# Performance work log

Hardware: AMD Instinct MI355X
Metric: run time of the kernel (lower is better)

Reference implementation:

```python
import jax, jax.numpy as jnp
import numpy as np

EPS_OT = 0.05
SINK_ITERS = 3
HEADS = 8


def _l2norm(x, axis):
    n = jnp.sqrt(jnp.sum(x * x, axis=axis, keepdims=True))
    return x / jnp.maximum(n, 1e-12)


def _conv(x, w, b, pad):
    y = jax.lax.conv_general_dilated(x, w, (1, 1), [(pad, pad), (pad, pad)],
                                     dimension_numbers=('NCHW', 'OIHW', 'NCHW'))
    return y + b[None, :, None, None]


def _bn(x, g, b):
    # BatchNorm2d in training mode: batch statistics over (B,H,W)
    m = jnp.mean(x, axis=(0, 2, 3), keepdims=True)
    v = jnp.var(x, axis=(0, 2, 3), keepdims=True)
    return (x - m) / jnp.sqrt(v + 1e-5) * g[None, :, None, None] + b[None, :, None, None]


def setup_inputs() -> dict:
    key = jax.random.key(0)
    ks = jax.random.split(key, 16)
    B, C, H, W = 2, 256, 64, 64
    TXT = 512
    rn = lambda k, shp, s=0.02: jax.random.normal(k, shp, dtype=jnp.float32) * s
    return {
        'img_feat': jax.random.normal(ks[0], (B, C, H, W), jnp.float32),
        'txt_feat': jax.random.normal(ks[1], (B, TXT), jnp.float32),
        'density_map': jax.random.uniform(ks[2], (B, 1, H, W), dtype=jnp.float32),
        'tp_w': rn(ks[3], (C, TXT)), 'tp_b': jnp.zeros((C,), jnp.float32),
        'wq': rn(ks[4], (C, C)), 'bq': jnp.zeros((C,), jnp.float32),
        'wk': rn(ks[5], (C, C)), 'bk': jnp.zeros((C,), jnp.float32),
        'wv': rn(ks[6], (C, C)), 'bv': jnp.zeros((C,), jnp.float32),
        'wo': rn(ks[7], (C, C)), 'bo': jnp.zeros((C,), jnp.float32),
        'ln_g': jnp.ones((C,), jnp.float32), 'ln_b': jnp.zeros((C,), jnp.float32),
        'op_w': rn(ks[8], (C, C, 1, 1)), 'op_b': jnp.zeros((C,), jnp.float32),
        'hm1_w': rn(ks[9], (C // 2, C, 3, 3)), 'hm1_b': jnp.zeros((C // 2,), jnp.float32),
        'hm_bn_g': jnp.ones((C // 2,), jnp.float32), 'hm_bn_b': jnp.zeros((C // 2,), jnp.float32),
        'hm2_w': rn(ks[10], (2, C // 2, 1, 1)), 'hm2_b': jnp.zeros((2,), jnp.float32),
        'hv1_w': rn(ks[11], (C // 2, C, 3, 3)), 'hv1_b': jnp.zeros((C // 2,), jnp.float32),
        'hv_bn_g': jnp.ones((C // 2,), jnp.float32), 'hv_bn_b': jnp.zeros((C // 2,), jnp.float32),
        'hv2_w': rn(ks[12], (2, C // 2, 1, 1)), 'hv2_b': jnp.zeros((2,), jnp.float32),
        'temperature': jnp.ones((1,), jnp.float32) * 0.07,
    }


def reference(img_feat, txt_feat, density_map, tp_w, tp_b, wq, bq, wk, bk, wv, bv,
              wo, bo, ln_g, ln_b, op_w, op_b, hm1_w, hm1_b, hm_bn_g, hm_bn_b,
              hm2_w, hm2_b, hv1_w, hv1_b, hv_bn_g, hv_bn_b, hv2_w, hv2_b, temperature):
    B, C, H, W = img_feat.shape
    N = H * W
    dh = C // HEADS

    # text projection -> single token [B,1,C]
    txt_emb = (txt_feat @ tp_w.T + tp_b)[:, None, :]
    img_flat = img_feat.reshape(B, C, N).transpose(0, 2, 1)  # [B,N,C]

    # multihead cross-attention, kv length 1
    q = (img_flat @ wq.T + bq).reshape(B, N, HEADS, dh)
    k = (txt_emb @ wk.T + bk).reshape(B, 1, HEADS, dh)
    v = (txt_emb @ wv.T + bv).reshape(B, 1, HEADS, dh)
    scores = jnp.einsum('bnhd,bmhd->bhnm', q, k) / np.float32(np.sqrt(dh))
    w_attn = jax.nn.softmax(scores, axis=-1)
    attn_out = jnp.einsum('bhnm,bmhd->bnhd', w_attn, v).reshape(B, N, C) @ wo.T + bo

    # residual + layernorm
    x = img_flat + attn_out
    mu = jnp.mean(x, axis=-1, keepdims=True)
    var = jnp.var(x, axis=-1, keepdims=True)
    source = (x - mu) / jnp.sqrt(var + 1e-5) * ln_g + ln_b  # [B,N,C]
    mod_img = source.transpose(0, 2, 1).reshape(B, C, H, W)

    # target marginal from density map
    target = jax.nn.relu(density_map.reshape(B, N)) + 1e-6
    q_marg = target / jnp.sum(target, axis=1, keepdims=True)

    # source marginal from cosine similarity to text
    img_n = _l2norm(mod_img, 1)
    txt_n = _l2norm(txt_emb[:, 0, :], 1)  # [B,C]
    cos = jnp.einsum('bchw,bc->bhw', img_n, txt_n).reshape(B, N)
    temp = jnp.maximum(temperature, 0.01)
    p_marg = jax.nn.softmax(cos / temp, axis=1)

    # Sinkhorn OT over NxN cosine cost
    sn = _l2norm(source, 2)
    sim = jnp.einsum('bnc,bmc->bnm', sn, sn)
    K = jnp.exp(-(1.0 - sim) / EPS_OT)
    u = jnp.ones_like(p_marg)
    vv = jnp.ones_like(q_marg)
    for _ in range(SINK_ITERS):
        vv = q_marg / (jnp.einsum('bnm,bn->bm', K, u) + 1e-8)
        u = p_marg / (jnp.einsum('bnm,bm->bn', K, vv) + 1e-8)
    T = u[:, :, None] * K * vv[:, None, :]
    fused = jnp.einsum('bnm,bnc->bmc', T, source)  # T^T @ source

    fused_feat = fused.transpose(0, 2, 1).reshape(B, C, H, W)
    out_feat = img_feat + _conv(fused_feat, op_w, op_b, 0)

    hm = _conv(jax.nn.relu(_bn(_conv(out_feat, hm1_w, hm1_b, 1), hm_bn_g, hm_bn_b)), hm2_w, hm2_b, 0)
    hv = _conv(jax.nn.relu(_bn(_conv(out_feat, hv1_w, hv1_b, 1), hv_bn_g, hv_bn_b)), hv2_w, hv2_b, 0)
    return (out_feat, hm, hv)
```

## Files before the change

kernel.cpp:

```cpp
#include <hip/hip_runtime.h>

#define B_ 2
#define C_ 256
#define N_ 4096
#define TXT_ 512
#define CH_ 128
#define TN 32
#define KSPLIT 4
#define PXR 4224
#define PXPAD 96
#define PXTOT (PXR + 2 * PXPAD)
#define L2E 28.853900817779268f

typedef unsigned short u16;
typedef unsigned char u8;
typedef __attribute__((ext_vector_type(8))) short short8;
typedef __attribute__((ext_vector_type(4))) float f32x4;
typedef __attribute__((ext_vector_type(2))) float f32x2;

__device__ __forceinline__ float bf2f(u16 v){
  union { unsigned u; float f; } w; w.u = ((unsigned)v) << 16; return w.f;
}
__device__ __forceinline__ u16 f2bf(float f){
  union { float f; unsigned u; } w; w.f = f;
  unsigned r = w.u + 0x7fffu + ((w.u >> 16) & 1u);
  return (u16)(r >> 16);
}

#define MFMA_BF16(a,b,c) __builtin_amdgcn_mfma_f32_16x16x32_bf16(a,b,c,0,0,0)

__device__ __forceinline__ void stage_tile(const u16* __restrict__ g, int stride, u16* lds, int t)
{
  #pragma unroll
  for (int q = 0; q < 4; q++){
    int e = q * 256 + t;
    int row = e >> 3;
    int slot = e & 7;
    const u16* gp = g + (size_t)row * stride + ((slot ^ (row & 7)) << 3);
    u16* lp = lds + (size_t)e * 8;
    __builtin_amdgcn_global_load_lds((const __attribute__((address_space(1))) void*)gp,
                                     (__attribute__((address_space(3))) void*)lp, 16, 0, 0);
  }
}

__device__ __forceinline__ void stage_tile512_256(const u16* __restrict__ g, int stride, u16* lds, int t)
{
  #pragma unroll
  for (int q = 0; q < 4; q++){
    int e = q * 512 + t;
    int row = e >> 3;
    int slot = e & 7;
    const u16* gp = g + (size_t)row * stride + ((slot ^ (row & 7)) << 3);
    u16* lp = lds + (size_t)e * 8;
    __builtin_amdgcn_global_load_lds((const __attribute__((address_space(1))) void*)gp,
                                     (__attribute__((address_space(3))) void*)lp, 16, 0, 0);
  }
}

__device__ __forceinline__ short8 frag_ld(const u16* lds, int row, int slot)
{
  return *(const short8*)(lds + row * 64 + ((slot ^ (row & 7)) << 3));
}

__global__ __launch_bounds__(256) void k_text(
    const float* __restrict__ txt, const float* __restrict__ tpw,
    const float* __restrict__ tpb, const float* __restrict__ wv,
    const float* __restrict__ bv, const float* __restrict__ wo,
    const float* __restrict__ bo,
    float* __restrict__ txt_emb, float* __restrict__ attn_c, float* __restrict__ txt_n)
{
  int b = blockIdx.x, t = threadIdx.x;
  __shared__ float te[C_], vs[C_], red[C_];
  const float* tb = txt + b * TXT_;
  const float* wr = tpw + (size_t)t * TXT_;
  float s = 0.f;
  for (int j = 0; j < TXT_; j++) s += tb[j] * wr[j];
  s += tpb[t];
  te[t] = s;
  txt_emb[b * C_ + t] = s;
  __syncthreads();
  float sv = 0.f;
  const float* wvr = wv + (size_t)t * C_;
  for (int j = 0; j < C_; j++) sv += te[j] * wvr[j];
  sv += bv[t];
  vs[t] = sv;
  __syncthreads();
  float sa = 0.f;
  const float* wor = wo + (size_t)t * C_;
  for (int j = 0; j < C_; j++) sa += vs[j] * wor[j];
  sa += bo[t];
  attn_c[b * C_ + t] = sa;
  red[t] = te[t] * te[t];
  __syncthreads();
  for (int o = 128; o > 0; o >>= 1){ if (t < o) red[t] += red[t + o]; __syncthreads(); }
  float nrm = sqrtf(red[0]);
  float inv = 1.f / fmaxf(nrm, 1e-12f);
  txt_n[b * C_ + t] = te[t] * inv;
}

__global__ __launch_bounds__(256) void k_source(
    const float* __restrict__ img, const float* __restrict__ attn_c,
    const float* __restrict__ ln_g, const float* __restrict__ ln_b,
    const float* __restrict__ txt_n,
    u16* __restrict__ srcT, u16* __restrict__ snb, float* __restrict__ cosv)
{
  int b = blockIdx.y;
  int n0 = blockIdx.x * TN;
  int t = threadIdx.x;
  __shared__ float x[C_][TN + 1];
  __shared__ float ps[8][TN];
  __shared__ float ps2[8][TN];
  __shared__ float ac_s[C_], g_s[C_], bb_s[C_], tn_s[C_];
  __shared__ float mean_s[TN], rstd_s[TN], rn_s[TN];
  ac_s[t] = attn_c[b * C_ + t];
  g_s[t]  = ln_g[t];
  bb_s[t] = ln_b[t];
  tn_s[t] = txt_n[b * C_ + t];
  const float* ib = img + (size_t)b * C_ * N_ + n0;
  for (int k = 0; k < TN; k++){
    int e = t + k * 256;
    int c = e >> 5, nn = e & 31;
    x[c][nn] = ib[(size_t)c * N_ + nn];
  }
  __syncthreads();
  for (int k = 0; k < TN; k++){
    int e = t + k * 256;
    int c = e >> 5, nn = e & 31;
    x[c][nn] += ac_s[c];
  }
  __syncthreads();
  {
    int p = t >> 5, nn = t & 31;
    float s1 = 0.f, s2 = 0.f;
    for (int j = 0; j < 32; j++){
      float v = x[p + 8 * j][nn];
      s1 += v; s2 += v * v;
    }
    ps[p][nn] = s1; ps2[p][nn] = s2;
  }
  __syncthreads();
  if (t < TN){
    float S1 = 0.f, S2 = 0.f;
    for (int pp = 0; pp < 8; pp++){ S1 += ps[pp][t]; S2 += ps2[pp][t]; }
    float mean = S1 * (1.f / C_);
    float var = S2 * (1.f / C_) - mean * mean;
    mean_s[t] = mean;
    rstd_s[t] = rsqrtf(var + 1e-5f);
  }
  __syncthreads();
  for (int k = 0; k < TN; k++){
    float sval = (x[t][k] - mean_s[k]) * rstd_s[k] * g_s[t] + bb_s[t];
    x[t][k] = sval;
  }
  for (int kq = 0; kq < TN; kq += 4){
    ushort4 pkv;
    pkv.x = f2bf(x[t][kq + 0]);
    pkv.y = f2bf(x[t][kq + 1]);
    pkv.z = f2bf(x[t][kq + 2]);
    pkv.w = f2bf(x[t][kq + 3]);
    *reinterpret_cast<ushort4*>(&srcT[(size_t)(b * C_ + t) * N_ + n0 + kq]) = pkv;
  }
  __syncthreads();
  {
    int p = t >> 5, nn = t & 31;
    float s2 = 0.f, sd = 0.f;
    for (int j = 0; j < 32; j++){
      int c = p + 8 * j;
      float v = x[c][nn];
      s2 += v * v; sd += v * tn_s[c];
    }
    ps[p][nn] = s2; ps2[p][nn] = sd;
  }
  __syncthreads();
  if (t < TN){
    float S2 = 0.f, SD = 0.f;
    for (int pp = 0; pp < 8; pp++){ S2 += ps[pp][t]; SD += ps2[pp][t]; }
    float nrm = sqrtf(S2);
    float rn = 1.f / fmaxf(nrm, 1e-12f);
    rn_s[t] = rn;
    cosv[(b << 12) + n0 + t] = SD * rn;
  }
  __syncthreads();
  for (int k = 0; k < TN; k++){
    snb[(size_t)((b << 12) + n0 + k) * C_ + t] = f2bf(x[t][k] * rn_s[k]);
  }
}

__global__ __launch_bounds__(256) void k_qmarg(const float* __restrict__ dens, float* __restrict__ q){
  int b = blockIdx.x, t = threadIdx.x;
  __shared__ float red[256];
  const float* d = dens + (size_t)b * N_;
  float s = 0.f;
  for (int n = t; n < N_; n += 256) s += fmaxf(d[n], 0.f) + 1e-6f;
  red[t] = s; __syncthreads();
  for (int o = 128; o > 0; o >>= 1){ if (t < o) red[t] += red[t + o]; __syncthreads(); }
  float inv = 1.f / red[0];
  for (int n = t; n < N_; n += 256) q[b * N_ + n] = (fmaxf(d[n], 0.f) + 1e-6f) * inv;
}

__global__ __launch_bounds__(256) void k_pmarg(const float* __restrict__ cosv,
    const float* __restrict__ temp_p, float* __restrict__ p){
  int b = blockIdx.x, t = threadIdx.x;
  __shared__ float red[256];
  float temp = fmaxf(temp_p[0], 0.01f);
  float inv_t = 1.f / temp;
  const float* cb = cosv + (size_t)b * N_;
  float m = -1e30f;
  for (int n = t; n < N_; n += 256) m = fmaxf(m, cb[n] * inv_t);
  red[t] = m; __syncthreads();
  for (int o = 128; o > 0; o >>= 1){ if (t < o) red[t] = fmaxf(red[t], red[t + o]); __syncthreads(); }
  m = red[0]; __syncthreads();
  float s = 0.f;
  for (int n = t; n < N_; n += 256) s += expf(cb[n] * inv_t - m);
  red[t] = s; __syncthreads();
  for (int o = 128; o > 0; o >>= 1){ if (t < o) red[t] += red[t + o]; __syncthreads(); }
  float invs = 1.f / red[0];
  for (int n = t; n < N_; n += 256) p[b * N_ + n] = expf(cb[n] * inv_t - m) * invs;
}

__global__ __launch_bounds__(256) void k_zero(float* __restrict__ p, int n){
  int i = blockIdx.x * 256 + threadIdx.x;
  if (i < n) p[i] = 0.f;
}

__global__ __launch_bounds__(256) void k_kgen(
    const u16* __restrict__ snb, u8* __restrict__ Kp, float* __restrict__ colsum)
{
  int b = blockIdx.z;
  int m0 = blockIdx.x << 7, n0 = blockIdx.y << 7;
  int t = threadIdx.x;
  int lane = t & 63, w = t >> 6;
  int wr = w >> 1, wc = w & 1;
  __shared__ __align__(16) u16 shbuf[128 * 128];
  u16* Al = shbuf;
  u16* Bl = shbuf + 128 * 64;
  __shared__ float cs[128];
  if (t < 128) cs[t] = 0.f;
  f32x4 zero = {0.f, 0.f, 0.f, 0.f};
  f32x4 acc[4][4];
  #pragma unroll
  for (int i = 0; i < 4; i++){
    #pragma unroll
    for (int j = 0; j < 4; j++) acc[i][j] = zero;
  }
  const u16* sb = snb + (size_t)b * N_ * C_;
  const u16* ga = sb + (size_t)m0 * C_;
  const u16* gb = sb + (size_t)n0 * C_;
  for (int kt = 0; kt < C_; kt += 64){
    stage_tile(ga + kt, C_, Al, t);
    stage_tile(gb + kt, C_, Bl, t);
    __syncthreads();
    #pragma unroll
    for (int kh = 0; kh < 2; kh++){
      short8 af[4], bfv[4];
      #pragma unroll
      for (int i = 0; i < 4; i++){
        af[i]  = frag_ld(Al, wr * 64 + i * 16 + (lane & 15), kh * 4 + (lane >> 4));
        bfv[i] = frag_ld(Bl, wc * 64 + i * 16 + (lane & 15), kh * 4 + (lane >> 4));
      }
      #pragma unroll
      for (int i = 0; i < 4; i++){
        #pragma unroll
        for (int j = 0; j < 4; j++)
          acc[i][j] = MFMA_BF16(af[i], bfv[j], acc[i][j]);
      }
    }
    __syncthreads();
  }
  u8* CtT = (u8*)shbuf;
  #pragma unroll
  for (int j = 0; j < 4; j++){
    int col = wc * 64 + j * 16 + (lane & 15);
    float csum = 0.f;
    #pragma unroll
    for (int i = 0; i < 4; i++){
      int rb = wr * 64 + i * 16 + (lane >> 4) * 4;
      float e0 = __builtin_amdgcn_exp2f(fmaf(acc[i][j][0], L2E, -L2E));
      float e1 = __builtin_amdgcn_exp2f(fmaf(acc[i][j][1], L2E, -L2E));
      float e2 = __builtin_amdgcn_exp2f(fmaf(acc[i][j][2], L2E, -L2E));
      float e3 = __builtin_amdgcn_exp2f(fmaf(acc[i][j][3], L2E, -L2E));
      int pk = __builtin_amdgcn_cvt_pk_fp8_f32(e0, e1, 0, false);
      pk = __builtin_amdgcn_cvt_pk_fp8_f32(e2, e3, pk, true);
      f32x2 d0 = __builtin_amdgcn_cvt_pk_f32_fp8(pk, false);
      f32x2 d1 = __builtin_amdgcn_cvt_pk_f32_fp8(pk, true);
      csum += (d0.x + d0.y) + (d1.x + d1.y);
      int wq = rb >> 2;
      *reinterpret_cast<unsigned*>(CtT + col * 128 + ((wq ^ ((col & 7) << 2)) << 2)) = (unsigned)pk;
    }
    atomicAdd(&cs[col], csum);
  }
  __syncthreads();
  u8* Kb = Kp + (size_t)b * N_ * N_;
  for (int e = t; e < 1024; e += 256){
    int row = e >> 3, un = e & 7;
    uint4 v = *(const uint4*)(CtT + row * 128 + ((un ^ (row & 7)) << 4));
    *reinterpret_cast<uint4*>(&Kb[(size_t)(n0 + row) * N_ + m0 + (un << 4)]) = v;
  }
  if (t < 128) atomicAdd(&colsum[b * N_ + n0 + t], cs[t]);
}

__global__ __launch_bounds__(256) void k_div(
    const float* __restrict__ marg, const float* __restrict__ denom, float* __restrict__ outp){
  int i = blockIdx.x * 256 + threadIdx.x;
  if (i < B_ * N_) outp[i] = marg[i] / (denom[i] + 1e-8f);
}

__global__ __launch_bounds__(256) void k_mv(
    const u8* __restrict__ Kp, const float* __restrict__ x,
    const float* __restrict__ marg, float* __restrict__ outp)
{
  int r0 = blockIdx.x * 8;
  int b = r0 >> 12;
  int t = threadIdx.x, w = t >> 6, lane = t & 63;
  __shared__ __align__(16) float xs[N_];
  const float* xb = x + b * N_;
  for (int i = t; i < N_ / 4; i += 256)
    reinterpret_cast<float4*>(xs)[i] = reinterpret_cast<const float4*>(xb)[i];
  __syncthreads();
  int r = r0 + w * 2;
  const u8* Kr0 = Kp + (size_t)b * N_ * N_ + (size_t)(r & (N_ - 1)) * N_;
  const u8* Kr1 = Kr0 + N_;
  float acc0 = 0.f, acc1 = 0.f;
  #pragma unroll
  for (int p = 0; p < 4; p++){
    int idx = p * 1024 + lane * 16;
    uint4 a = *reinterpret_cast<const uint4*>(Kr0 + idx);
    uint4 c = *reinterpret_cast<const uint4*>(Kr1 + idx);
    #pragma unroll
    for (int q = 0; q < 4; q++){
      unsigned aw = (q == 0) ? a.x : (q == 1) ? a.y : (q == 2) ? a.z : a.w;
      unsigned cw = (q == 0) ? c.x : (q == 1) ? c.y : (q == 2) ? c.z : c.w;
      float4 xv = *reinterpret_cast<const float4*>(xs + idx + q * 4);
      f32x2 al = __builtin_amdgcn_cvt_pk_f32_fp8((int)aw, false);
      f32x2 ah = __builtin_amdgcn_cvt_pk_f32_fp8((int)aw, true);
      f32x2 cl = __builtin_amdgcn_cvt_pk_f32_fp8((int)cw, false);
      f32x2 ch = __builtin_amdgcn_cvt_pk_f32_fp8((int)cw, true);
      acc0 += al.x * xv.x + al.y * xv.y + ah.x * xv.z + ah.y * xv.w;
      acc1 += cl.x * xv.x + cl.y * xv.y + ch.x * xv.z + ch.y * xv.w;
    }
  }
  for (int o = 32; o > 0; o >>= 1){
    acc0 += __shfl_down(acc0, o);
    acc1 += __shfl_down(acc1, o);
  }
  if (lane == 0){
    outp[r] = marg[r] / (acc0 + 1e-8f);
    outp[r + 1] = marg[r + 1] / (acc1 + 1e-8f);
  }
}

__global__ __launch_bounds__(256) void k_uscale(
    const u16* __restrict__ srcT, const float* __restrict__ uu, u16* __restrict__ usrcT)
{
  int i = blockIdx.x * 256 + threadIdx.x;
  int n8 = i & (N_ / 8 - 1);
  int row = i >> 9;
  int b = row >> 8;
  const u16* s = srcT + (size_t)row * N_ + n8 * 8;
  short8 v = *reinterpret_cast<const short8*>(s);
  const float* ub = uu + b * N_ + n8 * 8;
  short8 o;
  #pragma unroll
  for (int q = 0; q < 8; q++) o[q] = (short)f2bf(bf2f((u16)v[q]) * ub[q]);
  *reinterpret_cast<short8*>(usrcT + (size_t)row * N_ + n8 * 8) = o;
}

__global__ __launch_bounds__(512) void k_full(
    const u8* __restrict__ Kp, const u16* __restrict__ usrcT,
    const float* __restrict__ vvv,
    u16* __restrict__ p0, u16* __restrict__ p1,
    u16* __restrict__ p2, u16* __restrict__ p3)
{
  int m0 = blockIdx.x << 6;
  int b = blockIdx.z >> 2, ks = blockIdx.z & 3;
  int t = threadIdx.x, lane = t & 63, w = t >> 6;
  __shared__ __align__(16) u16 shbuf[64 * 64 + 256 * 64];
  __shared__ float vsm[64];
  u16* Al = shbuf;
  u16* Bl = shbuf + 64 * 64;
  if (t < 64) vsm[t] = vvv[b * N_ + m0 + t];
  f32x4 zero = {0.f, 0.f, 0.f, 0.f};
  f32x4 acc[4][2];
  #pragma unroll
  for (int i = 0; i < 4; i++){
    #pragma unroll
    for (int j = 0; j < 2; j++) acc[i][j] = zero;
  }
  const u8* ka = Kp + (size_t)b * N_ * N_ + (size_t)m0 * N_ + ks * (N_ / KSPLIT);
  const u16* ub = usrcT + (size_t)b * C_ * N_ + ks * (N_ / KSPLIT);
  for (int kt = 0; kt < N_ / KSPLIT; kt += 64){
    {
      int row = t >> 3, slot = t & 7;
      const u8* gp = ka + (size_t)row * N_ + kt + ((slot ^ (row & 7)) << 3);
      uint2 v8 = *reinterpret_cast<const uint2*>(gp);
      f32x2 q0 = __builtin_amdgcn_cvt_pk_f32_fp8((int)v8.x, false);
      f32x2 q1 = __builtin_amdgcn_cvt_pk_f32_fp8((int)v8.x, true);
      f32x2 q2 = __builtin_amdgcn_cvt_pk_f32_fp8((int)v8.y, false);
      f32x2 q3 = __builtin_amdgcn_cvt_pk_f32_fp8((int)v8.y, true);
      union { short8 s; unsigned u[4]; } o;
      asm("v_cvt_pk_bf16_f32 %0, %1, %2" : "=v"(o.u[0]) : "v"(q0.x), "v"(q0.y));
      asm("v_cvt_pk_bf16_f32 %0, %1, %2" : "=v"(o.u[1]) : "v"(q1.x), "v"(q1.y));
      asm("v_cvt_pk_bf16_f32 %0, %1, %2" : "=v"(o.u[2]) : "v"(q2.x), "v"(q2.y));
      asm("v_cvt_pk_bf16_f32 %0, %1, %2" : "=v"(o.u[3]) : "v"(q3.x), "v"(q3.y));
      *reinterpret_cast<short8*>(Al + (size_t)t * 8) = o.s;
    }
    stage_tile512_256(ub + kt, N_, Bl, t);
    __syncthreads();
    #pragma unroll
    for (int kh = 0; kh < 2; kh++){
      short8 af[4], bfv[2];
      #pragma unroll
      for (int i = 0; i < 4; i++)
        af[i] = frag_ld(Al, i * 16 + (lane & 15), kh * 4 + (lane >> 4));
      #pragma unroll
      for (int j = 0; j < 2; j++)
        bfv[j] = frag_ld(Bl, w * 32 + j * 16 + (lane & 15), kh * 4 + (lane >> 4));
      #pragma unroll
      for (int i = 0; i < 4; i++){
        #pragma unroll
        for (int j = 0; j < 2; j++)
          acc[i][j] = MFMA_BF16(af[i], bfv[j], acc[i][j]);
      }
    }
    __syncthreads();
  }
  u16* Ct = shbuf;
  #pragma unroll
  for (int j = 0; j < 2; j++){
    int col = w * 32 + j * 16 + (lane & 15);
    #pragma unroll
    for (int i = 0; i < 4; i++){
      int rb = i * 16 + (lane >> 4) * 4;
      #pragma unroll
      for (int r = 0; r < 4; r++){
        int row = rb + r;
        Ct[row * 256 + ((((col >> 3) ^ (row & 7)) << 3) | (col & 7))] =
            f2bf(acc[i][j][r] * vsm[row]);
      }
    }
  }
  __syncthreads();
  u16* P = (ks == 0) ? p0 : (ks == 1) ? p1 : (ks == 2) ? p2 : p3;
  for (int e = t; e < 2048; e += 512){
    int row = e >> 5, un = e & 31;
    short8 v8 = *(const short8*)(Ct + row * 256 + ((un ^ (row & 7)) << 3));
    *reinterpret_cast<short8*>(&P[(size_t)((b << 12) + m0 + row) * C_ + (un << 3)]) = v8;
  }
}

__global__ __launch_bounds__(256) void k_wcast(const float* __restrict__ w, u16* __restrict__ o){
  int i = blockIdx.x * 256 + threadIdx.x;
  o[i] = f2bf(w[i]);
}

__global__ __launch_bounds__(256) void k_opconv(
    const u16* __restrict__ opwB, const float* __restrict__ opb,
    const u16* __restrict__ p0, const u16* __restrict__ p1,
    const u16* __restrict__ p2, const u16* __restrict__ p3,
    const float* __restrict__ img, float* __restrict__ outf)
{
  int b = blockIdx.z;
  int n0 = blockIdx.x << 6;
  int co0 = blockIdx.y << 7;
  int t = threadIdx.x, lane = t & 63, w = t >> 6;
  int wr = w >> 1, wc = w & 1;
  __shared__ __align__(16) u16 Al[128 * 64];
  __shared__ __align__(16) u16 Bl[64 * 64];
  f32x4 zero = {0.f, 0.f, 0.f, 0.f};
  f32x4 acc[4][2];
  #pragma unroll
  for (int i = 0; i < 4; i++){
    #pragma unroll
    for (int j = 0; j < 2; j++) acc[i][j] = zero;
  }
  for (int ct = 0; ct < C_; ct += 64){
    stage_tile(opwB + (size_t)co0 * C_ + ct, C_, Al, t);
    #pragma unroll
    for (int q = 0; q < 2; q++){
      int e = q * 256 + t;
      int row = e >> 3, slot = e & 7;
      int col = ct + ((slot ^ (row & 7)) << 3);
      size_t idx = (size_t)((b << 12) + n0 + row) * C_ + col;
      short8 a0 = *reinterpret_cast<const short8*>(p0 + idx);
      short8 a1 = *reinterpret_cast<const short8*>(p1 + idx);
      short8 a2 = *reinterpret_cast<const short8*>(p2 + idx);
      short8 a3 = *reinterpret_cast<const short8*>(p3 + idx);
      short8 o;
      #pragma unroll
      for (int k = 0; k < 8; k++)
        o[k] = (short)f2bf(bf2f((u16)a0[k]) + bf2f((u16)a1[k]) + bf2f((u16)a2[k]) + bf2f((u16)a3[k]));
      *reinterpret_cast<short8*>(Bl + (size_t)e * 8) = o;
    }
    __syncthreads();
    #pragma unroll
    for (int kh = 0; kh < 2; kh++){
      short8 af[4], bfv[2];
      #pragma unroll
      for (int i = 0; i < 4; i++)
        af[i] = frag_ld(Al, wr * 64 + i * 16 + (lane & 15), kh * 4 + (lane >> 4));
      #pragma unroll
      for (int j = 0; j < 2; j++)
        bfv[j] = frag_ld(Bl, wc * 32 + j * 16 + (lane & 15), kh * 4 + (lane >> 4));
      #pragma unroll
      for (int i = 0; i < 4; i++){
        #pragma unroll
        for (int j = 0; j < 2; j++)
          acc[i][j] = MFMA_BF16(af[i], bfv[j], acc[i][j]);
      }
    }
    __syncthreads();
  }
  #pragma unroll
  for (int i = 0; i < 4; i++){
    int cb = co0 + wr * 64 + i * 16 + (lane >> 4) * 4;
    #pragma unroll
    for (int j = 0; j < 2; j++){
      int nc = n0 + wc * 32 + j * 16 + (lane & 15);
      #pragma unroll
      for (int r = 0; r < 4; r++){
        int co = cb + r;
        size_t oi = (size_t)(b * C_ + co) * N_ + nc;
        outf[oi] = acc[i][j][r] + img[oi] + opb[co];
      }
    }
  }
}

__global__ __launch_bounds__(256) void k_tr(const float* __restrict__ outf, u16* __restrict__ inTp)
{
  int b = blockIdx.z;
  int c0 = blockIdx.y << 6;
  int px0 = blockIdx.x << 6;
  int t = threadIdx.x;
  __shared__ float tile[64][65];
  int tx = t & 63, ty4 = t >> 6;
  for (int cc = ty4; cc < 64; cc += 4)
    tile[cc][tx] = outf[((size_t)(b * C_) + c0 + cc) * N_ + px0 + tx];
  __syncthreads();
  int p = t >> 2, cg = (t & 3) << 4;
  int px = px0 + p;
  int y = px >> 6, x = px & 63;
  int pxp = y * 66 + x + 1;
  u16* dst = inTp + ((size_t)b * PXTOT + PXPAD + pxp) * C_ + c0 + cg;
  #pragma unroll
  for (int q = 0; q < 16; q += 4){
    ushort4 pk;
    pk.x = f2bf(tile[cg + q + 0][p]);
    pk.y = f2bf(tile[cg + q + 1][p]);
    pk.z = f2bf(tile[cg + q + 2][p]);
    pk.w = f2bf(tile[cg + q + 3][p]);
    *reinterpret_cast<ushort4*>(dst + q) = pk;
  }
}

__global__ __launch_bounds__(256) void k_wtr(
    const float* __restrict__ hm1_w, const float* __restrict__ hv1_w,
    const float* __restrict__ hm1_b, const float* __restrict__ hv1_b,
    u16* __restrict__ Wt, float* __restrict__ biasF)
{
  int i = blockIdx.x * 256 + threadIdx.x;
  int ci = i & 255, co = (i >> 8) & 255, tap = i >> 16;
  float v = (co < CH_) ? hm1_w[((size_t)co * C_ + ci) * 9 + tap]
                       : hv1_w[((size_t)(co - CH_) * C_ + ci) * 9 + tap];
  Wt[i] = f2bf(v);
  if (i < CH_) biasF[i] = hm1_b[i];
  else if (i < 2 * CH_) biasF[i] = hv1_b[i - CH_];
}

__global__ __launch_bounds__(256) void k_conv3m(
    const u16* __restrict__ inTp, const u16* __restrict__ Wt,
    const float* __restrict__ biasF,
    u16* __restrict__ q0, u16* __restrict__ q1,
    u16* __restrict__ q2, u16* __restrict__ q3)
{
  int px0 = blockIdx.x << 7;
  int cot = blockIdx.y;
  int b = blockIdx.z >> 2, ks = blockIdx.z & 3;
  int t = threadIdx.x, lane = t & 63, w = t >> 6;
  int wr = w >> 1, wc = w & 1;
  __shared__ __align__(16) u16 Al[128 * 64];
  __shared__ __align__(16) u16 Bl[128 * 64];
  f32x4 zero = {0.f, 0.f, 0.f, 0.f};
  f32x4 acc[4][4];
  #pragma unroll
  for (int i = 0; i < 4; i++){
    #pragma unroll
    for (int j = 0; j < 4; j++) acc[i][j] = zero;
  }
  const u16* inb = inTp + ((size_t)b * PXTOT + PXPAD + px0) * C_;
  for (int s = ks * 9; s < ks * 9 + 9; s++){
    int tap = s >> 2, cic = (s & 3) << 6;
    int ky = tap / 3, kx = tap - ky * 3;
    int off = (ky - 1) * 66 + (kx - 1);
    stage_tile(Wt + ((size_t)tap * 256 + cot * 128) * C_ + cic, C_, Al, t);
    stage_tile(inb + (ptrdiff_t)off * C_ + cic, C_, Bl, t);
    __syncthreads();
    #pragma unroll
    for (int kh = 0; kh < 2; kh++){
      short8 af[4], bfv[4];
      #pragma unroll
      for (int i = 0; i < 4; i++){
        af[i]  = frag_ld(Al, wr * 64 + i * 16 + (lane & 15), kh * 4 + (lane >> 4));
        bfv[i] = frag_ld(Bl, wc * 64 + i * 16 + (lane & 15), kh * 4 + (lane >> 4));
      }
      #pragma unroll
      for (int i = 0; i < 4; i++){
        #pragma unroll
        for (int j = 0; j < 4; j++)
          acc[i][j] = MFMA_BF16(af[i], bfv[j], acc[i][j]);
      }
    }
    __syncthreads();
  }
  u16* P = (ks == 0) ? q0 : (ks == 1) ? q1 : (ks == 2) ? q2 : q3;
  #pragma unroll
  for (int i = 0; i < 4; i++){
    #pragma unroll
    for (int j = 0; j < 4; j++){
      int pxp = px0 + wc * 64 + j * 16 + (lane & 15);
      int y = pxp / 66;
      int xm = pxp - y * 66;
      bool valid = (xm >= 1 && xm <= 64);
      int outn = y * 64 + xm - 1;
      #pragma unroll
      for (int r = 0; r < 4; r++){
        int co = cot * 128 + wr * 64 + i * 16 + (lane >> 4) * 4 + r;
        if (valid){
          float bco = (ks == 0) ? biasF[co] : 0.f;
          P[((size_t)(b * 256 + co)) * N_ + outn] = f2bf(acc[i][j][r] + bco);
        }
      }
    }
  }
}

__global__ __launch_bounds__(256) void k_bnstats2(
    const u16* __restrict__ p0, const u16* __restrict__ p1,
    const u16* __restrict__ p2, const u16* __restrict__ p3,
    float* __restrict__ stats)
{
  int ch = blockIdx.x, t = threadIdx.x;
  __shared__ float r1[256], r2[256];
  float s1 = 0.f, s2 = 0.f;
  for (int i = t; i < B_ * N_; i += 256){
    int b = i >> 12, n = i & (N_ - 1);
    size_t idx = ((size_t)(b * 256 + ch)) * N_ + n;
    float v = bf2f(p0[idx]) + bf2f(p1[idx]) + bf2f(p2[idx]) + bf2f(p3[idx]);
    s1 += v; s2 += v * v;
  }
  r1[t] = s1; r2[t] = s2; __syncthreads();
  for (int o = 128; o > 0; o >>= 1){
    if (t < o){ r1[t] += r1[t + o]; r2[t] += r2[t + o]; }
    __syncthreads();
  }
  if (t == 0){
    float mean = r1[0] / (float)(B_ * N_);
    float var = r2[0] / (float)(B_ * N_) - mean * mean;
    stats[ch * 2] = mean;
    stats[ch * 2 + 1] = rsqrtf(var + 1e-5f);
  }
}

__global__ __launch_bounds__(256) void k_headF(
    const u16* __restrict__ p0, const u16* __restrict__ p1,
    const u16* __restrict__ p2, const u16* __restrict__ p3,
    const float* __restrict__ stats,
    const float* __restrict__ hm_g, const float* __restrict__ hm_b,
    const float* __restrict__ hm2_w, const float* __restrict__ hm2_b,
    const float* __restrict__ hv_g, const float* __restrict__ hv_b,
    const float* __restrict__ hv2_w, const float* __restrict__ hv2_b,
    float* __restrict__ outhm, float* __restrict__ outhv)
{
  int t = threadIdx.x;
  int nl = t & 31, g = t >> 5;
  int idx0 = blockIdx.x * 32;
  int idx = idx0 + nl;
  int b = idx >> 12, n = idx & (N_ - 1);
  int head = g >> 2;
  int ch0 = (g & 3) * 32;
  const float* gg = head ? hv_g : hm_g;
  const float* gb = head ? hv_b : hm_b;
  const float* w2 = head ? hv2_w : hm2_w;
  float a0 = 0.f, a1 = 0.f;
  #pragma unroll 8
  for (int cc = 0; cc < 32; cc++){
    int ch = ch0 + cc;
    int fc = head * CH_ + ch;
    size_t id = ((size_t)(b * 256 + fc)) * N_ + n;
    float v = bf2f(p0[id]) + bf2f(p1[id]) + bf2f(p2[id]) + bf2f(p3[id]);
    float rr = fmaxf((v - stats[fc * 2]) * stats[fc * 2 + 1] * gg[ch] + gb[ch], 0.f);
    a0 += w2[ch] * rr;
    a1 += w2[CH_ + ch] * rr;
  }
  __shared__ float r0[8][32], r1[8][32];
  r0[g][nl] = a0; r1[g][nl] = a1;
  __syncthreads();
  if (t < 64){
    int hh = t >> 5, n2 = t & 31;
    int base = hh * 4;
    float s0 = r0[base][n2] + r0[base + 1][n2] + r0[base + 2][n2] + r0[base + 3][n2];
    float s1 = r1[base][n2] + r1[base + 1][n2] + r1[base + 2][n2] + r1[base + 3][n2];
    int idx2 = idx0 + n2;
    int b2 = idx2 >> 12, nn = idx2 & (N_ - 1);
    float* op = hh ? outhv : outhm;
    const float* bp = hh ? hv2_b : hm2_b;
    op[(size_t)(b2 * 2) * N_ + nn] = s0 + bp[0];
    op[(size_t)(b2 * 2 + 1) * N_ + nn] = s1 + bp[1];
  }
}

extern "C" void kernel_launch(void* const* d_in, const int* in_sizes, int n_in,
                              void* d_out, int out_size, void* d_ws, size_t ws_size,
                              hipStream_t stream)
{
  const float* img   = (const float*)d_in[0];
  const float* txt   = (const float*)d_in[1];
  const float* dens  = (const float*)d_in[2];
  const float* tp_w  = (const float*)d_in[3];
  const float* tp_b  = (const float*)d_in[4];
  const float* wv    = (const float*)d_in[9];
  const float* bv    = (const float*)d_in[10];
  const float* wo    = (const float*)d_in[11];
  const float* bo    = (const float*)d_in[12];
  const float* ln_g  = (const float*)d_in[13];
  const float* ln_b  = (const float*)d_in[14];
  const float* op_w  = (const float*)d_in[15];
  const float* op_b  = (const float*)d_in[16];
  const float* hm1_w = (const float*)d_in[17];
  const float* hm1_b = (const float*)d_in[18];
  const float* hm_g  = (const float*)d_in[19];
  const float* hm_b  = (const float*)d_in[20];
  const float* hm2_w = (const float*)d_in[21];
  const float* hm2_b = (const float*)d_in[22];
  const float* hv1_w = (const float*)d_in[23];
  const float* hv1_b = (const float*)d_in[24];
  const float* hv_g  = (const float*)d_in[25];
  const float* hv_b  = (const float*)d_in[26];
  const float* hv2_w = (const float*)d_in[27];
  const float* hv2_b = (const float*)d_in[28];
  const float* temp  = (const float*)d_in[29];

  char* wsb = (char*)d_ws;
  size_t off = 0;
  auto alloc = [&](size_t bytes) -> void* {
    void* p = wsb + off;
    off += (bytes + 255) & ~(size_t)255;
    return p;
  };
  u8*    Km     = (u8*)   alloc((size_t)B_ * N_ * N_ * sizeof(u8));
  u16*   snb16  = (u16*)  alloc((size_t)B_ * N_ * C_ * sizeof(u16));
  u16*   srcT16 = (u16*)  alloc((size_t)B_ * C_ * N_ * sizeof(u16));
  u16*   usrcT  = (u16*)  alloc((size_t)B_ * C_ * N_ * sizeof(u16));
  u16*   part1  = (u16*)  alloc((size_t)B_ * N_ * C_ * sizeof(u16));
  u16*   part2  = (u16*)  alloc((size_t)B_ * N_ * C_ * sizeof(u16));
  u16*   part3  = (u16*)  alloc((size_t)B_ * N_ * C_ * sizeof(u16));
  u16*   inTp   = (u16*)  alloc((size_t)B_ * PXTOT * C_ * sizeof(u16));
  u16*   Wt     = (u16*)  alloc((size_t)9 * 256 * C_ * sizeof(u16));
  u16*   opwB   = (u16*)  alloc((size_t)C_ * C_ * sizeof(u16));
  float* biasF  = (float*)alloc(256 * sizeof(float));
  float* txt_emb= (float*)alloc(B_ * C_ * sizeof(float));
  float* attn_c = (float*)alloc(B_ * C_ * sizeof(float));
  float* txt_n  = (float*)alloc(B_ * C_ * sizeof(float));
  float* cosv   = (float*)alloc(B_ * N_ * sizeof(float));
  float* qm     = (float*)alloc(B_ * N_ * sizeof(float));
  float* pm     = (float*)alloc(B_ * N_ * sizeof(float));
  float* uu     = (float*)alloc(B_ * N_ * sizeof(float));
  float* vvv    = (float*)alloc(B_ * N_ * sizeof(float));
  float* colsum = (float*)alloc(B_ * N_ * sizeof(float));
  float* stats  = (float*)alloc(256 * 2 * sizeof(float));

  u16* part0 = snb16;

  float* outf  = (float*)d_out;
  float* outhm = outf + (size_t)B_ * C_ * N_;
  float* outhv = outhm + (size_t)B_ * 2 * N_;

  k_text<<<B_, 256, 0, stream>>>(txt, tp_w, tp_b, wv, bv, wo, bo, txt_emb, attn_c, txt_n);
  k_source<<<dim3(N_ / TN, B_), 256, 0, stream>>>(img, attn_c, ln_g, ln_b, txt_n, srcT16, snb16, cosv);
  k_qmarg<<<B_, 256, 0, stream>>>(dens, qm);
  k_pmarg<<<B_, 256, 0, stream>>>(cosv, temp, pm);
  k_zero<<<(B_ * N_ + 255) / 256, 256, 0, stream>>>(colsum, B_ * N_);
  k_wtr<<<9 * 256, 256, 0, stream>>>(hm1_w, hv1_w, hm1_b, hv1_b, Wt, biasF);
  k_wcast<<<C_ * C_ / 256, 256, 0, stream>>>(op_w, opwB);
  k_zero<<<((int)((size_t)B_ * PXTOT * C_ / 2) + 255) / 256, 256, 0, stream>>>((float*)inTp, (int)((size_t)B_ * PXTOT * C_ / 2));
  k_kgen<<<dim3(N_ / 128, N_ / 128, B_), 256, 0, stream>>>(snb16, Km, colsum);
  k_div<<<(B_ * N_ + 255) / 256, 256, 0, stream>>>(qm, colsum, vvv);
  k_mv<<<B_ * N_ / 8, 256, 0, stream>>>(Km, vvv, pm, uu);
  k_mv<<<B_ * N_ / 8, 256, 0, stream>>>(Km, uu, qm, vvv);
  k_mv<<<B_ * N_ / 8, 256, 0, stream>>>(Km, vvv, pm, uu);
  k_mv<<<B_ * N_ / 8, 256, 0, stream>>>(Km, uu, qm, vvv);
  k_mv<<<B_ * N_ / 8, 256, 0, stream>>>(Km, vvv, pm, uu);
  k_uscale<<<(B_ * C_ * N_ / 8 + 255) / 256, 256, 0, stream>>>(srcT16, uu, usrcT);
  k_full<<<dim3(N_ / 64, 1, B_ * KSPLIT), 512, 0, stream>>>(Km, usrcT, vvv, part0, part1, part2, part3);
  k_opconv<<<dim3(N_ / 64, C_ / 128, B_), 256, 0, stream>>>(opwB, op_b, part0, part1, part2, part3, img, outf);
  k_tr<<<dim3(N_ / 64, 4, B_), 256, 0, stream>>>(outf, inTp);
  k_conv3m<<<dim3(33, 2, B_ * KSPLIT), 256, 0, stream>>>(inTp, Wt, biasF, part0, part1, part2, part3);
  k_bnstats2<<<256, 256, 0, stream>>>(part0, part1, part2, part3, stats);
  k_headF<<<B_ * N_ / 32, 256, 0, stream>>>(part0, part1, part2, part3, stats,
      hm_g, hm_b, hm2_w, hm2_b, hv_g, hv_b, hv2_w, hv2_b, outhm, outhv);
}
```

Baseline: 242.4 us.

## Parallelize text projection across blocks and halve conv3 pixel tile

The single two-block text kernel, which did serial per-thread dot products, is split in two. The first kernel spreads the 512-wide projection over 128 blocks using wave-level shuffle reductions. The second computes the V/O projections and norm with 1024 threads and coalesced float4 loads. The 3x3 conv kernel now uses a 64-pixel tile instead of 128, doubling the grid to fill more CUs at the cost of reloading the weight tile twice as often.

```diff
diff --git a/kernel.cpp b/kernel.cpp
--- a/kernel.cpp
+++ b/kernel.cpp
@@ -43,6 +43,20 @@
   }
 }
 
+__device__ __forceinline__ void stage_tile256_64(const u16* __restrict__ g, int stride, u16* lds, int t)
+{
+  #pragma unroll
+  for (int q = 0; q < 2; q++){
+    int e = q * 256 + t;
+    int row = e >> 3;
+    int slot = e & 7;
+    const u16* gp = g + (size_t)row * stride + ((slot ^ (row & 7)) << 3);
+    u16* lp = lds + (size_t)e * 8;
+    __builtin_amdgcn_global_load_lds((const __attribute__((address_space(1))) void*)gp,
+                                     (__attribute__((address_space(3))) void*)lp, 16, 0, 0);
+  }
+}
+
 __device__ __forceinline__ void stage_tile512_256(const u16* __restrict__ g, int stride, u16* lds, int t)
 {
   #pragma unroll
@@ -62,40 +76,69 @@
   return *(const short8*)(lds + row * 64 + ((slot ^ (row & 7)) << 3));
 }
 
-__global__ __launch_bounds__(256) void k_text(
+__global__ __launch_bounds__(256) void k_text1(
     const float* __restrict__ txt, const float* __restrict__ tpw,
-    const float* __restrict__ tpb, const float* __restrict__ wv,
+    const float* __restrict__ tpb, float* __restrict__ te)
+{
+  int b = blockIdx.y;
+  int ch = blockIdx.x * 4 + (threadIdx.x >> 6);
+  int lane = threadIdx.x & 63;
+  const float* tb = txt + (size_t)b * TXT_;
+  const float* wr = tpw + (size_t)ch * TXT_;
+  float4 a0 = *reinterpret_cast<const float4*>(wr + lane * 4);
+  float4 a1 = *reinterpret_cast<const float4*>(wr + 256 + lane * 4);
+  float4 b0 = *reinterpret_cast<const float4*>(tb + lane * 4);
+  float4 b1 = *reinterpret_cast<const float4*>(tb + 256 + lane * 4);
+  float s = a0.x * b0.x + a0.y * b0.y + a0.z * b0.z + a0.w * b0.w
+          + a1.x * b1.x + a1.y * b1.y + a1.z * b1.z + a1.w * b1.w;
+  for (int o = 32; o > 0; o >>= 1) s += __shfl_down(s, o);
+  if (lane == 0) te[b * C_ + ch] = s + tpb[ch];
+}
+
+__global__ __launch_bounds__(1024) void k_text2(
+    const float* __restrict__ te, const float* __restrict__ wv,
     const float* __restrict__ bv, const float* __restrict__ wo,
     const float* __restrict__ bo,
-    float* __restrict__ txt_emb, float* __restrict__ attn_c, float* __restrict__ txt_n)
+    float* __restrict__ attn_c, float* __restrict__ txt_n)
 {
   int b = blockIdx.x, t = threadIdx.x;
-  __shared__ float te[C_], vs[C_], red[C_];
-  const float* tb = txt + b * TXT_;
-  const float* wr = tpw + (size_t)t * TXT_;
-  float s = 0.f;
-  for (int j = 0; j < TXT_; j++) s += tb[j] * wr[j];
-  s += tpb[t];
-  te[t] = s;
-  txt_emb[b * C_ + t] = s;
-  __syncthreads();
-  float sv = 0.f;
-  const float* wvr = wv + (size_t)t * C_;
-  for (int j = 0; j < C_; j++) sv += te[j] * wvr[j];
-  sv += bv[t];
-  vs[t] = sv;
-  __syncthreads();
-  float sa = 0.f;
-  const float* wor = wo + (size_t)t * C_;
-  for (int j = 0; j < C_; j++) sa += vs[j] * wor[j];
-  sa += bo[t];
-  attn_c[b * C_ + t] = sa;
-  red[t] = te[t] * te[t];
-  __syncthreads();
-  for (int o = 128; o > 0; o >>= 1){ if (t < o) red[t] += red[t + o]; __syncthreads(); }
-  float nrm = sqrtf(red[0]);
-  float inv = 1.f / fmaxf(nrm, 1e-12f);
-  txt_n[b * C_ + t] = te[t] * inv;
+  int w = t >> 6, lane = t & 63;
+  __shared__ float te_s[C_], vs_s[C_];
+  __shared__ float red[16];
+  __shared__ float inv_s;
+  if (t < C_) te_s[t] = te[b * C_ + t];
+  __syncthreads();
+  {
+    float nv = (t < C_) ? te_s[t] * te_s[t] : 0.f;
+    for (int o = 32; o > 0; o >>= 1) nv += __shfl_down(nv, o);
+    if (lane == 0) red[w] = nv;
+  }
+  __syncthreads();
+  if (t == 0){
+    float S = 0.f;
+    for (int q = 0; q < 16; q++) S += red[q];
+    inv_s = 1.f / fmaxf(sqrtf(S), 1e-12f);
+  }
+  #pragma unroll
+  for (int r = 0; r < 16; r++){
+    int ch = r * 16 + w;
+    float4 av = *reinterpret_cast<const float4*>(wv + (size_t)ch * C_ + lane * 4);
+    float s = av.x * te_s[lane * 4] + av.y * te_s[lane * 4 + 1]
+            + av.z * te_s[lane * 4 + 2] + av.w * te_s[lane * 4 + 3];
+    for (int o = 32; o > 0; o >>= 1) s += __shfl_down(s, o);
+    if (lane == 0) vs_s[ch] = s + bv[ch];
+  }
+  __syncthreads();
+  #pragma unroll
+  for (int r = 0; r < 16; r++){
+    int ch = r * 16 + w;
+    float4 av = *reinterpret_cast<const float4*>(wo + (size_t)ch * C_ + lane * 4);
+    float s = av.x * vs_s[lane * 4] + av.y * vs_s[lane * 4 + 1]
+            + av.z * vs_s[lane * 4 + 2] + av.w * vs_s[lane * 4 + 3];
+    for (int o = 32; o > 0; o >>= 1) s += __shfl_down(s, o);
+    if (lane == 0) attn_c[b * C_ + ch] = s + bo[ch];
+  }
+  if (t < C_) txt_n[b * C_ + t] = te_s[t] * inv_s;
 }
 
 __global__ __launch_bounds__(256) void k_source(
@@ -573,19 +616,19 @@
     u16* __restrict__ q0, u16* __restrict__ q1,
     u16* __restrict__ q2, u16* __restrict__ q3)
 {
-  int px0 = blockIdx.x << 7;
+  int px0 = blockIdx.x << 6;
   int cot = blockIdx.y;
   int b = blockIdx.z >> 2, ks = blockIdx.z & 3;
   int t = threadIdx.x, lane = t & 63, w = t >> 6;
   int wr = w >> 1, wc = w & 1;
   __shared__ __align__(16) u16 Al[128 * 64];
-  __shared__ __align__(16) u16 Bl[128 * 64];
+  __shared__ __align__(16) u16 Bl[64 * 64];
   f32x4 zero = {0.f, 0.f, 0.f, 0.f};
-  f32x4 acc[4][4];
+  f32x4 acc[4][2];
   #pragma unroll
   for (int i = 0; i < 4; i++){
     #pragma unroll
-    for (int j = 0; j < 4; j++) acc[i][j] = zero;
+    for (int j = 0; j < 2; j++) acc[i][j] = zero;
   }
   const u16* inb = inTp + ((size_t)b * PXTOT + PXPAD + px0) * C_;
   for (int s = ks * 9; s < ks * 9 + 9; s++){
@@ -593,20 +636,21 @@
     int ky = tap / 3, kx = tap - ky * 3;
     int off = (ky - 1) * 66 + (kx - 1);
     stage_tile(Wt + ((size_t)tap * 256 + cot * 128) * C_ + cic, C_, Al, t);
-    stage_tile(inb + (ptrdiff_t)off * C_ + cic, C_, Bl, t);
+    stage_tile256_64(inb + (ptrdiff_t)off * C_ + cic, C_, Bl, t);
     __syncthreads();
     #pragma unroll
     for (int kh = 0; kh < 2; kh++){
-      short8 af[4], bfv[4];
-      #pragma unroll
-      for (int i = 0; i < 4; i++){
-        af[i]  = frag_ld(Al, wr * 64 + i * 16 + (lane & 15), kh * 4 + (lane >> 4));
-        bfv[i] = frag_ld(Bl, wc * 64 + i * 16 + (lane & 15), kh * 4 + (lane >> 4));
-      }
+      short8 af[4], bfv[2];
+      #pragma unroll
+      for (int i = 0; i < 4; i++)
+        af[i] = frag_ld(Al, wr * 64 + i * 16 + (lane & 15), kh * 4 + (lane >> 4));
+      #pragma unroll
+      for (int j = 0; j < 2; j++)
+        bfv[j] = frag_ld(Bl, wc * 32 + j * 16 + (lane & 15), kh * 4 + (lane >> 4));
       #pragma unroll
       for (int i = 0; i < 4; i++){
         #pragma unroll
-        for (int j = 0; j < 4; j++)
+        for (int j = 0; j < 2; j++)
           acc[i][j] = MFMA_BF16(af[i], bfv[j], acc[i][j]);
       }
     }
@@ -616,8 +660,8 @@
   #pragma unroll
   for (int i = 0; i < 4; i++){
     #pragma unroll
-    for (int j = 0; j < 4; j++){
-      int pxp = px0 + wc * 64 + j * 16 + (lane & 15);
+    for (int j = 0; j < 2; j++){
+      int pxp = px0 + wc * 32 + j * 16 + (lane & 15);
       int y = pxp / 66;
       int xm = pxp - y * 66;
       bool valid = (xm >= 1 && xm <= 64);
@@ -758,7 +802,7 @@
   u16*   Wt     = (u16*)  alloc((size_t)9 * 256 * C_ * sizeof(u16));
   u16*   opwB   = (u16*)  alloc((size_t)C_ * C_ * sizeof(u16));
   float* biasF  = (float*)alloc(256 * sizeof(float));
-  float* txt_emb= (float*)alloc(B_ * C_ * sizeof(float));
+  float* teb    = (float*)alloc(B_ * C_ * sizeof(float));
   float* attn_c = (float*)alloc(B_ * C_ * sizeof(float));
   float* txt_n  = (float*)alloc(B_ * C_ * sizeof(float));
   float* cosv   = (float*)alloc(B_ * N_ * sizeof(float));
@@ -775,7 +819,8 @@
   float* outhm = outf + (size_t)B_ * C_ * N_;
   float* outhv = outhm + (size_t)B_ * 2 * N_;
 
-  k_text<<<B_, 256, 0, stream>>>(txt, tp_w, tp_b, wv, bv, wo, bo, txt_emb, attn_c, txt_n);
+  k_text1<<<dim3(64, B_), 256, 0, stream>>>(txt, tp_w, tp_b, teb);
+  k_text2<<<B_, 1024, 0, stream>>>(teb, wv, bv, wo, bo, attn_c, txt_n);
   k_source<<<dim3(N_ / TN, B_), 256, 0, stream>>>(img, attn_c, ln_g, ln_b, txt_n, srcT16, snb16, cosv);
   k_qmarg<<<B_, 256, 0, stream>>>(dens, qm);
   k_pmarg<<<B_, 256, 0, stream>>>(cosv, temp, pm);
@@ -794,7 +839,7 @@
   k_full<<<dim3(N_ / 64, 1, B_ * KSPLIT), 512, 0, stream>>>(Km, usrcT, vvv, part0, part1, part2, part3);
   k_opconv<<<dim3(N_ / 64, C_ / 128, B_), 256, 0, stream>>>(opwB, op_b, part0, part1, part2, part3, img, outf);
   k_tr<<<dim3(N_ / 64, 4, B_), 256, 0, stream>>>(outf, inTp);
-  k_conv3m<<<dim3(33, 2, B_ * KSPLIT), 256, 0, stream>>>(inTp, Wt, biasF, part0, part1, part2, part3);
+  k_conv3m<<<dim3(66, 2, B_ * KSPLIT), 256, 0, stream>>>(inTp, Wt, biasF, part0, part1, part2, part3);
   k_bnstats2<<<256, 256, 0, stream>>>(part0, part1, part2, part3, stats);
   k_headF<<<B_ * N_ / 32, 256, 0, stream>>>(part0, part1, part2, part3, stats,
       hm_g, hm_b, hm2_w, hm2_b, hv_g, hv_b, hv2_w, hv2_b, outhm, outhv);
```

Result: faster. 230.2 us (-5.0%).
